# Optimization experiments

Measured on AMD Instinct MI355X. Metric: run time of the kernel, lower is better.

## Reference

```python
import jax, jax.numpy as jnp
import numpy as np

B, C, H, W, OC, K = 8, 256, 120, 120, 256, 3


def setup_inputs() -> dict:
    key = jax.random.key(0)
    ks = jax.random.split(key, 6)
    x = jax.random.normal(ks[0], (B, C, H, W), jnp.float32)
    y = jax.random.normal(ks[1], (B, C, H, W), jnp.float32)
    # generate_kernel: 1x1 conv in_yC -> in_xC (weight stored as (out, in))
    gen_w = jax.random.normal(ks[2], (C, C), jnp.float32) * (1.0 / np.sqrt(C))
    gen_b = jax.random.normal(ks[3], (C,), jnp.float32) * 0.01
    # fuse: 3x3 conv in_xC -> out_C, padding 1
    fuse_w = jax.random.normal(ks[4], (OC, C, 3, 3), jnp.float32) * (1.0 / np.sqrt(C * 9))
    fuse_b = jax.random.normal(ks[5], (OC,), jnp.float32) * 0.01
    return {"x": x, "y": y, "gen_w": gen_w, "gen_b": gen_b,
            "fuse_w": fuse_w, "fuse_b": fuse_b}


def reference(x, y, gen_w, gen_b, fuse_w, fuse_b):
    b, c, h, w = x.shape
    # AdaptiveAvgPool2d(K): H,W divisible by K -> uniform average pooling
    yp = y.reshape(b, c, K, h // K, K, w // K).mean(axis=(3, 5))  # (B,C,K,K)
    # 1x1 conv to generate per-sample per-channel kernels
    kernel = jnp.einsum('oc,bcij->boij', gen_w, yp) + gen_b[None, :, None, None]
    # dynamic depthwise conv: groups = B*C, padding 1 (cross-correlation, as torch)
    xg = x.reshape(1, b * c, h, w)
    kg = kernel.reshape(b * c, 1, K, K)
    dn = jax.lax.conv_dimension_numbers(xg.shape, kg.shape, ('NCHW', 'OIHW', 'NCHW'))
    out = jax.lax.conv_general_dilated(
        xg, kg, window_strides=(1, 1), padding=((1, 1), (1, 1)),
        dimension_numbers=dn, feature_group_count=b * c)
    out = out.reshape(b, c, h, w)
    # fuse: dense 3x3 conv C -> OC, padding 1, with bias
    dn2 = jax.lax.conv_dimension_numbers(out.shape, fuse_w.shape, ('NCHW', 'OIHW', 'NCHW'))
    res = jax.lax.conv_general_dilated(
        out, fuse_w, window_strides=(1, 1), padding=((1, 1), (1, 1)),
        dimension_numbers=dn2)
    return res + fuse_b[None, :, None, None]
```

## Files before the change

### kernel.cpp

```cpp
#include <hip/hip_runtime.h>
#include <hip/hip_bf16.h>
#include <stdint.h>

#define TB 8
#define TC 256
#define TH 120
#define TW 120
#define THW 14400
#define TOC 256
#define PH 122
#define PW 122

typedef short bf16x8 __attribute__((ext_vector_type(8)));
typedef float f32x4 __attribute__((ext_vector_type(4)));

#define OUTP_BYTES ((size_t)TB * PH * PW * TC * 2)
#define YP_OFF     OUTP_BYTES
#define DK_OFF     (YP_OFF + (size_t)TB * TC * 9 * 4)
#define WP_OFF     (DK_OFF + (size_t)TB * TC * 9 * 4)

__global__ void zero_halo_kernel(char* __restrict__ outP) {
    int i = blockIdx.x * 256 + threadIdx.x;
    int pos_idx = i >> 5, part = i & 31;
    int b = pos_idx / 484; int k = pos_idx - b * 484;
    int h, w;
    if (k < 122)      { h = 0;   w = k; }
    else if (k < 244) { h = 121; w = k - 122; }
    else { int m = k - 244; h = 1 + (m >> 1); w = (m & 1) ? 121 : 0; }
    size_t pos = ((size_t)b * PH + h) * PW + w;
    uint4 z; z.x = 0u; z.y = 0u; z.z = 0u; z.w = 0u;
    *(uint4*)(outP + pos * 512 + part * 16) = z;
}

__global__ __launch_bounds__(128) void pool_kernel(const float* __restrict__ y,
                                                   float* __restrict__ yp) {
    int bc = blockIdx.x, t = threadIdx.x;
    __shared__ float pr[120][4];
    __shared__ float p2[9][8];
    const float* src = y + (size_t)bc * THW;
    if (t < 120) {
        const float4* row = (const float4*)(src + t * TW);
        float s0 = 0.f, s1 = 0.f, s2 = 0.f;
        #pragma unroll
        for (int j = 0; j < 10; ++j)  { float4 v = row[j]; s0 += (v.x + v.y) + (v.z + v.w); }
        #pragma unroll
        for (int j = 10; j < 20; ++j) { float4 v = row[j]; s1 += (v.x + v.y) + (v.z + v.w); }
        #pragma unroll
        for (int j = 20; j < 30; ++j) { float4 v = row[j]; s2 += (v.x + v.y) + (v.z + v.w); }
        pr[t][0] = s0; pr[t][1] = s1; pr[t][2] = s2;
    }
    __syncthreads();
    if (t < 72) {
        int bin = t >> 3, ch = t & 7;
        int bh = bin / 3, bw = bin - bh * 3;
        float a = 0.f;
        #pragma unroll
        for (int r = 0; r < 5; ++r) a += pr[bh * 40 + ch * 5 + r][bw];
        p2[bin][ch] = a;
    }
    __syncthreads();
    if (t < 9) {
        float a = 0.f;
        #pragma unroll
        for (int j = 0; j < 8; ++j) a += p2[t][j];
        yp[bc * 9 + t] = a * (1.f / 1600.f);
    }
}

__global__ void gen_kernel(const float* __restrict__ yp, const float* __restrict__ gen_w,
                           const float* __restrict__ gen_b, float* __restrict__ dk) {
    int b = blockIdx.x, t = threadIdx.x;
    __shared__ float yps[TC * 9];
    for (int i = t; i < TC * 9; i += 256) yps[i] = yp[b * TC * 9 + i];
    __syncthreads();
    float acc[9];
    float bias = gen_b[t];
    #pragma unroll
    for (int j = 0; j < 9; ++j) acc[j] = bias;
    for (int c = 0; c < TC; ++c) {
        float w = gen_w[t * TC + c];
        #pragma unroll
        for (int j = 0; j < 9; ++j) acc[j] += w * yps[c * 9 + j];
    }
    #pragma unroll
    for (int j = 0; j < 9; ++j) dk[(b * TC + t) * 9 + j] = acc[j];
}

__global__ __launch_bounds__(1024) void dw_kernel(const float* __restrict__ x,
        const float* __restrict__ dk, __hip_bfloat16* __restrict__ outP) {
    int bid = blockIdx.x;
    int hs = bid & 7;
    int cc = (bid >> 3) & 7;
    int b  = bid >> 6;
    int t = threadIdx.x;
    int c  = t >> 5;
    int wq = t & 31;
    bool active = wq < 30;
    int w0 = wq * 4;
    int cg = cc * 32 + c;
    const float* xp = x + (size_t)(b * TC + cg) * THW;
    const float* dkp = dk + (size_t)(b * TC + cg) * 9;
    float k0[3], k1[3], k2[3];
    #pragma unroll
    for (int j = 0; j < 3; ++j) { k0[j] = dkp[j]; k1[j] = dkp[3 + j]; k2[j] = dkp[6 + j]; }

    __shared__ __align__(16) __hip_bfloat16 stage[2][32][124];

    int h0 = hs * 15;
    float A[6], B[6], C[6];
    auto loadrow = [&](int hh, float* V) {
        if (hh < 0 || hh >= TH) {
            #pragma unroll
            for (int j = 0; j < 6; ++j) V[j] = 0.f;
            return;
        }
        const float* row = xp + hh * TW;
        float4 v = *(const float4*)(row + w0);
        V[1] = v.x; V[2] = v.y; V[3] = v.z; V[4] = v.w;
        V[0] = (wq > 0)  ? row[w0 - 1] : 0.f;
        V[5] = (wq < 29) ? row[w0 + 4] : 0.f;
    };
    if (active) { loadrow(h0 - 1, A); loadrow(h0, B); }

    for (int r = 0; r < 15; ++r) {
        int h = h0 + r;
        if (active) {
            loadrow(h + 1, C);
            ushort4 pk;
            #pragma unroll
            for (int i = 0; i < 4; ++i) {
                float o = A[i] * k0[0] + A[i + 1] * k0[1] + A[i + 2] * k0[2]
                        + B[i] * k1[0] + B[i + 1] * k1[1] + B[i + 2] * k1[2]
                        + C[i] * k2[0] + C[i + 1] * k2[1] + C[i + 2] * k2[2];
                __hip_bfloat16 hb = __float2bfloat16(o);
                ushort u = *(ushort*)&hb;
                if (i == 0) pk.x = u; else if (i == 1) pk.y = u;
                else if (i == 2) pk.z = u; else pk.w = u;
            }
            *(ushort4*)&stage[r & 1][c][w0] = pk;
            #pragma unroll
            for (int j = 0; j < 6; ++j) { A[j] = B[j]; B[j] = C[j]; }
        }
        __syncthreads();
        if (t < 480) {
            int w = t >> 2, part = t & 3;
            ushort vals[8];
            #pragma unroll
            for (int j = 0; j < 8; ++j) vals[j] = *(const ushort*)&stage[r & 1][part * 8 + j][w];
            uint4 o;
            o.x = (uint)vals[0] | ((uint)vals[1] << 16);
            o.y = (uint)vals[2] | ((uint)vals[3] << 16);
            o.z = (uint)vals[4] | ((uint)vals[5] << 16);
            o.w = (uint)vals[6] | ((uint)vals[7] << 16);
            size_t pos = ((size_t)b * PH + (h + 1)) * PW + (w + 1);
            *(uint4*)((char*)outP + pos * 512 + cc * 64 + part * 16) = o;
        }
    }
}

__global__ void wprep_kernel(const float* __restrict__ fuse_w, __hip_bfloat16* __restrict__ Wp) {
    int i = blockIdx.x * 256 + threadIdx.x;
    int ij = i >> 16;
    int oc = (i >> 8) & 255;
    int c  = i & 255;
    Wp[i] = __float2bfloat16(fuse_w[(oc * 256 + c) * 9 + ij]);
}

typedef const __attribute__((address_space(1))) char* gas_t;
typedef __attribute__((address_space(3))) char* las_t;
__device__ __forceinline__ void gload16(const char* g, char* l) {
    __builtin_amdgcn_global_load_lds((gas_t)g, (las_t)l, 16, 0, 0);
}
__device__ __forceinline__ void barrier_() {
    asm volatile("" ::: "memory");
    __builtin_amdgcn_s_barrier();
    asm volatile("" ::: "memory");
}

__global__ __launch_bounds__(512, 2) void gemm_kernel(
        const __hip_bfloat16* __restrict__ outP,
        const __hip_bfloat16* __restrict__ Wp,
        const float* __restrict__ fuse_b,
        float* __restrict__ res) {
    __shared__ __align__(16) char lds[2][65536];
    const int t = threadIdx.x;
    const int lane = t & 63;
    const int wv = t >> 6;
    const int wm = wv >> 2;
    const int wn = wv & 3;
    const int bm = blockIdx.x;

    const char* gI = (const char*)outP;
    const char* gW = (const char*)Wp;

    const int sw  = (lane & 7) << 4;
    const int klo = (lane >> 4) << 4;
    const int rowA0 = wm * 128 + (lane & 15);
    const int aA_k0 = rowA0 * 128 + (klo ^ sw);
    const int aA_k1 = rowA0 * 128 + ((64 + klo) ^ sw);
    const int rowB0 = wn * 64 + (lane & 15);
    const int aB_k0 = 32768 + rowB0 * 128 + (klo ^ sw);
    const int aB_k1 = 32768 + rowB0 * 128 + ((64 + klo) ^ sw);

    const int srb = (((lane & 7) ^ (lane >> 3)) << 4);
    int srcA[2][2], srcB[2][2];
    #pragma unroll
    for (int h = 0; h < 2; ++h) {
        #pragma unroll
        for (int r = 0; r < 2; ++r) {
            int p = r * 64 + wv * 8 + (lane >> 3);
            int m = bm * 256 + h * 128 + p;
            int b = m / THW; int rr = m - b * THW;
            int hh = rr / TW; int w = rr - hh * TW;
            srcA[h][r] = (((b * PH + hh) * PW + w) << 9) + srb;
            srcB[h][r] = ((h * 128 + p) << 9) + srb;
        }
    }

    bf16x8 rA[8], rB[8];
    f32x4 acc[8][4];
    #pragma unroll
    for (int f = 0; f < 8; ++f) {
        #pragma unroll
        for (int g = 0; g < 4; ++g) { f32x4 z = {0.f,0.f,0.f,0.f}; acc[f][g] = z; }
    }

    auto OFFI = [&](int s) {
        int ij = s >> 2; int di = ij / 3, dj = ij - di * 3;
        return ((di * PW + dj) << 9) + ((s & 3) << 7);
    };
    auto OFFW = [&](int s) {
        return ((s >> 2) << 17) + ((s & 3) << 7);
    };
    auto STA = [&](int buf, int h, int offI) {
        char* base = &lds[buf][h * 16384 + t * 16];
        gload16(gI + srcA[h][0] + offI, base);
        gload16(gI + srcA[h][1] + offI, base + 8192);
    };
    auto STB = [&](int buf, int h, int offW) {
        char* base = &lds[buf][32768 + h * 16384 + t * 16];
        gload16(gW + srcB[h][0] + offW, base);
        gload16(gW + srcB[h][1] + offW, base + 8192);
    };

#define DS_A(BUF, MH) \
    { _Pragma("unroll") for (int f = 0; f < 4; ++f) { \
        rA[f*2+0] = *(const bf16x8*)(&lds[BUF][0] + aA_k0 + (MH)*8192 + f*2048); \
        rA[f*2+1] = *(const bf16x8*)(&lds[BUF][0] + aA_k1 + (MH)*8192 + f*2048); } }
#define DS_B(BUF, OH) \
    { _Pragma("unroll") for (int g = 0; g < 2; ++g) { \
        rB[(OH)*4+g*2+0] = *(const bf16x8*)(&lds[BUF][0] + aB_k0 + (OH)*4096 + g*2048); \
        rB[(OH)*4+g*2+1] = *(const bf16x8*)(&lds[BUF][0] + aB_k1 + (OH)*4096 + g*2048); } }
#define MMA(MH, OH) \
    { __builtin_amdgcn_s_setprio(1); \
      _Pragma("unroll") for (int kk = 0; kk < 2; ++kk) \
        _Pragma("unroll") for (int f = 0; f < 4; ++f) \
          _Pragma("unroll") for (int g = 0; g < 2; ++g) \
            acc[(MH)*4+f][(OH)*2+g] = __builtin_amdgcn_mfma_f32_16x16x32_bf16( \
                rB[(OH)*4+g*2+kk], rA[f*2+kk], acc[(MH)*4+f][(OH)*2+g], 0, 0, 0); \
      __builtin_amdgcn_s_setprio(0); }

    {
        int offI0 = OFFI(0), offW0 = OFFW(0), offW1 = OFFW(1);
        STA(0, 0, offI0); STA(0, 1, offI0);
        STB(0, 0, offW0); STB(0, 1, offW0);
        STB(1, 0, offW1); STB(1, 1, offW1);
    }
    asm volatile("s_waitcnt vmcnt(4)" ::: "memory");
    barrier_();

    #pragma unroll 1
    for (int it = 0; it < 18; ++it) {
        const int t1 = 2 * it + 1, t2 = 2 * it + 2, t3 = 2 * it + 3;
        const bool has2 = t2 < 36, has3 = t3 < 36;
        const int offI1 = OFFI(t1);
        const int offI2 = has2 ? OFFI(t2) : 0;
        const int offW2 = has2 ? OFFW(t2) : 0;
        const int offW3 = has3 ? OFFW(t3) : 0;

        DS_A(0, 0); DS_B(0, 0);
        STA(1, 0, offI1);
        barrier_(); MMA(0, 0); barrier_();
        DS_B(0, 1);
        STA(1, 1, offI1);
        barrier_(); MMA(0, 1); barrier_();
        DS_A(0, 1);
        if (has2) STB(0, 0, offW2);
        barrier_(); MMA(1, 0); barrier_();
        if (has2) STB(0, 1, offW2);
        if (it < 17) { asm volatile("s_waitcnt vmcnt(4)" ::: "memory"); }
        else         { asm volatile("s_waitcnt vmcnt(0)" ::: "memory"); }
        barrier_(); MMA(1, 1); barrier_();
        DS_A(1, 0); DS_B(1, 0);
        if (has2) STA(0, 0, offI2);
        barrier_(); MMA(0, 0); barrier_();
        DS_B(1, 1);
        if (has2) STA(0, 1, offI2);
        barrier_(); MMA(0, 1); barrier_();
        DS_A(1, 1);
        if (has3) STB(1, 0, offW3);
        barrier_(); MMA(1, 0); barrier_();
        if (has3) STB(1, 1, offW3);
        if (it < 17) { asm volatile("s_waitcnt vmcnt(4)" ::: "memory"); }
        else         { asm volatile("s_waitcnt vmcnt(0)" ::: "memory"); }
        barrier_(); MMA(1, 1); barrier_();
    }
#undef DS_A
#undef DS_B
#undef MMA

    int baseM[8];
    #pragma unroll
    for (int f = 0; f < 8; ++f) {
        int m = bm * 256 + wm * 128 + f * 16 + (lane & 15);
        int b = m / THW; int rr = m - b * THW;
        baseM[f] = b * (TOC * THW) + rr;
    }
    const int oc0 = wn * 64 + ((lane >> 4) << 2);
    float bias[4][4];
    #pragma unroll
    for (int g = 0; g < 4; ++g) {
        #pragma unroll
        for (int j = 0; j < 4; ++j) bias[g][j] = fuse_b[oc0 + g * 16 + j];
    }
    #pragma unroll
    for (int g = 0; g < 4; ++g) {
        #pragma unroll
        for (int f = 0; f < 8; ++f) {
            #pragma unroll
            for (int j = 0; j < 4; ++j)
                res[baseM[f] + (oc0 + g * 16 + j) * THW] = acc[f][g][j] + bias[g][j];
        }
    }
}

extern "C" void kernel_launch(void* const* d_in, const int* in_sizes, int n_in,
                              void* d_out, int out_size, void* d_ws, size_t ws_size,
                              hipStream_t stream) {
    const float* x      = (const float*)d_in[0];
    const float* y      = (const float*)d_in[1];
    const float* gen_w  = (const float*)d_in[2];
    const float* gen_b  = (const float*)d_in[3];
    const float* fuse_w = (const float*)d_in[4];
    const float* fuse_b = (const float*)d_in[5];
    float* out = (float*)d_out;
    char* ws = (char*)d_ws;

    __hip_bfloat16* outP = (__hip_bfloat16*)(ws);
    float* yp = (float*)(ws + YP_OFF);
    float* dk = (float*)(ws + DK_OFF);
    __hip_bfloat16* Wp = (__hip_bfloat16*)(ws + WP_OFF);

    zero_halo_kernel<<<484, 256, 0, stream>>>((char*)outP);
    pool_kernel<<<TB * TC, 128, 0, stream>>>(y, yp);
    gen_kernel<<<TB, 256, 0, stream>>>(yp, gen_w, gen_b, dk);
    wprep_kernel<<<2304, 256, 0, stream>>>(fuse_w, Wp);
    dw_kernel<<<512, 1024, 0, stream>>>(x, dk, outP);
    gemm_kernel<<<450, 512, 0, stream>>>(outP, Wp, fuse_b, out);
}
```

Measured before the change: 247.5 us.

## Restructure GEMM pipeline with full-tile prefetch and XCD-aware block remapping

Reworks the main GEMM loop so that each LDS buffer is computed over its full K tile before being refilled with the tile two steps ahead. Both tiles are prefetched in the prologue, and the wait allows up to eight loads in flight. The aim is to hide more global-load latency behind MFMA work. It also remaps blockIdx so that each XCD gets a contiguous range of M tiles, which is meant to improve L2 locality. The deeper prefetch keeps more loads outstanding, and the remap hardcodes a grid of 450 blocks.

Result: no change. 248.4 us (+0.4%).

```diff
diff --git a/kernel.cpp b/kernel.cpp
--- a/kernel.cpp
+++ b/kernel.cpp
@@ -188,7 +188,10 @@
     const int wv = t >> 6;
     const int wm = wv >> 2;
     const int wn = wv & 3;
-    const int bm = blockIdx.x;
+
+    const int orig = blockIdx.x;
+    const int xcd = orig & 7, lid = orig >> 3;
+    const int bm = (xcd < 2 ? xcd * 57 : 114 + (xcd - 2) * 56) + lid;
 
     const char* gI = (const char*)outP;
     const char* gW = (const char*)Wp;
@@ -260,51 +263,36 @@
                 rB[(OH)*4+g*2+kk], rA[f*2+kk], acc[(MH)*4+f][(OH)*2+g], 0, 0, 0); \
       __builtin_amdgcn_s_setprio(0); }
 
+    auto GROUP = [&](int buf, int stageT, int waitMode) {
+        DS_A(buf, 0); DS_B(buf, 0);
+        barrier_(); MMA(0, 0); barrier_();
+        DS_B(buf, 1);
+        barrier_(); MMA(0, 1); barrier_();
+        DS_A(buf, 1);
+        if (stageT >= 0) { int oW = OFFW(stageT); STB(buf, 0, oW); STB(buf, 1, oW); }
+        barrier_(); MMA(1, 0); barrier_();
+        if (stageT >= 0) { int oI = OFFI(stageT); STA(buf, 0, oI); STA(buf, 1, oI); }
+        barrier_(); MMA(1, 1);
+        if (waitMode == 0)      { asm volatile("s_waitcnt vmcnt(8)" ::: "memory"); }
+        else if (waitMode == 1) { asm volatile("s_waitcnt vmcnt(0)" ::: "memory"); }
+        barrier_();
+    };
+
     {
-        int offI0 = OFFI(0), offW0 = OFFW(0), offW1 = OFFW(1);
-        STA(0, 0, offI0); STA(0, 1, offI0);
-        STB(0, 0, offW0); STB(0, 1, offW0);
-        STB(1, 0, offW1); STB(1, 1, offW1);
-    }
-    asm volatile("s_waitcnt vmcnt(4)" ::: "memory");
+        int oI0 = OFFI(0), oW0 = OFFW(0), oI1 = OFFI(1), oW1 = OFFW(1);
+        STA(0, 0, oI0); STA(0, 1, oI0); STB(0, 0, oW0); STB(0, 1, oW0);
+        STA(1, 0, oI1); STA(1, 1, oI1); STB(1, 0, oW1); STB(1, 1, oW1);
+    }
+    asm volatile("s_waitcnt vmcnt(8)" ::: "memory");
     barrier_();
 
     #pragma unroll 1
-    for (int it = 0; it < 18; ++it) {
-        const int t1 = 2 * it + 1, t2 = 2 * it + 2, t3 = 2 * it + 3;
-        const bool has2 = t2 < 36, has3 = t3 < 36;
-        const int offI1 = OFFI(t1);
-        const int offI2 = has2 ? OFFI(t2) : 0;
-        const int offW2 = has2 ? OFFW(t2) : 0;
-        const int offW3 = has3 ? OFFW(t3) : 0;
-
-        DS_A(0, 0); DS_B(0, 0);
-        STA(1, 0, offI1);
-        barrier_(); MMA(0, 0); barrier_();
-        DS_B(0, 1);
-        STA(1, 1, offI1);
-        barrier_(); MMA(0, 1); barrier_();
-        DS_A(0, 1);
-        if (has2) STB(0, 0, offW2);
-        barrier_(); MMA(1, 0); barrier_();
-        if (has2) STB(0, 1, offW2);
-        if (it < 17) { asm volatile("s_waitcnt vmcnt(4)" ::: "memory"); }
-        else         { asm volatile("s_waitcnt vmcnt(0)" ::: "memory"); }
-        barrier_(); MMA(1, 1); barrier_();
-        DS_A(1, 0); DS_B(1, 0);
-        if (has2) STA(0, 0, offI2);
-        barrier_(); MMA(0, 0); barrier_();
-        DS_B(1, 1);
-        if (has2) STA(0, 1, offI2);
-        barrier_(); MMA(0, 1); barrier_();
-        DS_A(1, 1);
-        if (has3) STB(1, 0, offW3);
-        barrier_(); MMA(1, 0); barrier_();
-        if (has3) STB(1, 1, offW3);
-        if (it < 17) { asm volatile("s_waitcnt vmcnt(4)" ::: "memory"); }
-        else         { asm volatile("s_waitcnt vmcnt(0)" ::: "memory"); }
-        barrier_(); MMA(1, 1); barrier_();
-    }
+    for (int gg = 0; gg < 17; ++gg) {
+        GROUP(0, 2 * gg + 2, 0);
+        GROUP(1, 2 * gg + 3, 0);
+    }
+    GROUP(0, -1, 1);
+    GROUP(1, -1, 2);
 #undef DS_A
 #undef DS_B
 #undef MMA
```
